# Kernel tuning notes

Measured on AMD Instinct MI355X. Metric: run time of the kernel, lower is better.

The kernel has to match this reference:

```python
import jax, jax.numpy as jnp
import numpy as np

D = 1024          # input_dim
H = 16            # num_heads
S = 2             # scalar
MAX_LEN = 2048
HEAD_DIM = D // H // S      # 32
DV = D // H                 # 64, value head dim
SCALING = (D // H) ** -0.5


def setup_inputs() -> dict:
    key = jax.random.key(0)
    k1, k2, k3, k4, k5, k6 = jax.random.split(key, 6)
    L, B = 2046, 4
    input_tensor = jax.random.normal(k1, (L, B, D), dtype=jnp.float32)
    # k_v_proj: Linear(MAX_LEN, MAX_LEN // S); bias exists but is unused in forward
    w_kv = jax.random.normal(k2, (MAX_LEN // S, MAX_LEN), dtype=jnp.float32) / np.sqrt(MAX_LEN)
    # q_proj: Linear(D, D // S)
    w_q = jax.random.normal(k3, (D // S, D), dtype=jnp.float32) / np.sqrt(D)
    b_q = jax.random.normal(k4, (D // S,), dtype=jnp.float32) * 0.01
    # out_proj: Linear(D, D)
    w_out = jax.random.normal(k5, (D, D), dtype=jnp.float32) / np.sqrt(D)
    b_out = jax.random.normal(k6, (D,), dtype=jnp.float32) * 0.01
    return {"input_tensor": input_tensor, "w_kv": w_kv, "w_q": w_q,
            "b_q": b_q, "w_out": w_out, "b_out": b_out}


def reference(input_tensor, w_kv, w_q, b_q, w_out, b_out):
    L, B, _ = input_tensor.shape
    P = L // S + 1                       # projected (low-rank) sequence length
    X = jnp.transpose(input_tensor, (1, 0, 2))        # [B, L, D]
    q = X @ w_q.T + b_q                                # [B, L, D/S]
    Wp = w_kv.T[:L, :P]                                # [L, P] sequence projection
    v = jnp.einsum('bld,lp->bdp', X, Wp)               # [B, D, P]
    k = jnp.einsum('blc,lp->bcp', q, Wp)               # [B, D/S, P]
    q = q * SCALING
    # q: b l (h d) -> b h l d
    qh = q.reshape(B, L, H, HEAD_DIM).transpose(0, 2, 1, 3)
    # k: b (d h) p -> b h d p   (d outer, h inner in the channel split)
    kh = k.reshape(B, HEAD_DIM, H, P).transpose(0, 2, 1, 3)
    # v: b (d h) p -> b h p d
    vh = v.reshape(B, DV, H, P).transpose(0, 2, 3, 1)
    attn = jnp.einsum('bhld,bhdp->bhlp', qh, kh)       # [B, H, L, P]
    attn = jax.nn.softmax(attn.astype(jnp.float32), axis=-1).astype(attn.dtype)
    out = jnp.einsum('bhlp,bhpd->bhld', attn, vh)      # [B, H, L, DV]
    # (b h) l d -> b l (d h): d outer, h inner in concat
    out = out.transpose(0, 2, 3, 1).reshape(B, L, D)
    out = out @ w_out.T + b_out                        # [B, L, D]
    return jnp.transpose(out, (1, 0, 2))               # [L, B, D]
```

## Files before the change

kernel.cpp:

```cpp
#include <hip/hip_runtime.h>
#include <hip/hip_bf16.h>

typedef long long i64;
typedef unsigned int uint;
using u16 = unsigned short;
using f32x4  = __attribute__((ext_vector_type(4))) float;
using bf16x8 = __attribute__((ext_vector_type(8))) short;
using u32x4  = __attribute__((ext_vector_type(4))) uint;
using u16x4  = __attribute__((ext_vector_type(4))) u16;

#define QSCALE 0.18033688011112042f

#if __has_builtin(__builtin_amdgcn_exp2f)
#define EXP2(x) __builtin_amdgcn_exp2f(x)
#else
#define EXP2(x) __builtin_exp2f(x)
#endif

__device__ __forceinline__ u16 f2b(float x) {
    uint u = __float_as_uint(x);
    return (u16)((u + 0x7FFFu + ((u >> 16) & 1u)) >> 16);
}
__device__ __forceinline__ float b2f(u16 h) {
    return __uint_as_float((uint)h << 16);
}
__device__ __forceinline__ uint cvt_pk_bf16(float lo, float hi) {
    uint r;
    asm("v_cvt_pk_bf16_f32 %0, %1, %2" : "=v"(r) : "v"(lo), "v"(hi));
    return r;
}

__global__ __launch_bounds__(256) void conv_pad(
    const float* __restrict__ src, u16* __restrict__ dst,
    int M_valid, int K_valid, int kshift, int s_row)
{
    i64 i = (i64)blockIdx.x * 256 + threadIdx.x;
    int m = (int)(i >> (kshift - 2));
    int k = ((int)(i & ((1 << (kshift - 2)) - 1))) << 2;
    u16x4 hv;
    #pragma unroll
    for (int j = 0; j < 4; ++j) {
        int kk = k + j;
        float x = (m < M_valid && kk < K_valid) ? src[(i64)m * s_row + kk] : 0.f;
        hv[j] = f2b(x);
    }
    *(u16x4*)(dst + ((i64)m << kshift) + k) = hv;
}

__global__ __launch_bounds__(256) void conv_wout_perm(
    const float* __restrict__ w, u16* __restrict__ dst)
{
    int i = blockIdx.x * 256 + threadIdx.x;
    int n = i >> 8, kp4 = (i & 255) << 2;
    u16x4 hv;
    #pragma unroll
    for (int j = 0; j < 4; ++j) {
        int kp = kp4 + j;
        hv[j] = f2b(w[((i64)n << 10) + ((kp & 63) << 4) + (kp >> 6)]);
    }
    *(u16x4*)(dst + ((i64)n << 10) + kp4) = hv;
}

__global__ __launch_bounds__(256) void build_kvA(
    const u16* __restrict__ Xb, const u16* __restrict__ qu,
    u16* __restrict__ dst)
{
    const int b = blockIdx.z, r0 = blockIdx.y * 64, l0 = blockIdx.x * 64;
    const int tid = threadIdx.x;
    __shared__ float ts[64][65];
    #pragma unroll
    for (int t = 0; t < 16; ++t) {
        int idx = t * 256 + tid;
        int ch = idx & 63, lr = idx >> 6;
        int lg = l0 + lr;
        float v = 0.f;
        if (lg < 2046) {
            if (r0 < 1024) v = b2f(Xb[((i64)lg * 4 + b) * 1024 + (r0 + ch)]);
            else           v = b2f(qu[((i64)lg * 4 + b) * 512 + (r0 - 1024 + ch)]);
        }
        ts[lr][ch] = v;
    }
    __syncthreads();
    #pragma unroll
    for (int t = 0; t < 16; ++t) {
        int idx = t * 256 + tid;
        int ll = idx & 63, rl = idx >> 6;
        dst[((i64)b * 1536 + r0 + rl) * 2048 + l0 + ll] = f2b(ts[ll][rl]);
    }
}

template<int MODE>
__global__ __launch_bounds__(256) void gemm_bf16(
    const u16* __restrict__ A, i64 a_bs,
    const u16* __restrict__ Bm,
    float* __restrict__ C, const float* __restrict__ bias,
    u16* __restrict__ x0, u16* __restrict__ x1,
    int Krow, int KT, int M_valid)
{
    __shared__ __align__(16) u16 As[4096], Bs[8192];
    const int tid = threadIdx.x, lane = tid & 63, w = tid >> 6;
    const int fr = lane & 15, g = lane >> 4;

    const int fid = blockIdx.x;
    const int xcd = fid & 7, s = fid >> 3;
    int nb, mb, bz;
    if (MODE == 0)      { nb = s & 3; mb = xcd * 16 + (s >> 2); bz = 0; }
    else if (MODE == 1) { nb = s & 7; int pr = xcd * 12 + (s >> 3); bz = pr / 24; mb = pr % 24; }
    else                { nb = s & 7; int pr = xcd * 16 + (s >> 3); bz = pr >> 5; mb = pr & 31; }

    const int srow = tid >> 3, sch = tid & 7;
    const int scol = (sch ^ (srow & 7)) << 3;
    const u16* Asrc = A + (i64)bz * a_bs + ((i64)mb * 64 + srow) * Krow + scol;
    const u16* Bsrc = Bm + ((i64)nb * 128 + srow) * Krow + scol;
    char* Adst = (char*)As + srow * 128 + sch * 16;
    char* Bdst = (char*)Bs + srow * 128 + sch * 16;

    f32x4 acc[2][4];
    #pragma unroll
    for (int i = 0; i < 2; ++i)
        #pragma unroll
        for (int j = 0; j < 4; ++j)
            acc[i][j] = (f32x4){0.f, 0.f, 0.f, 0.f};

    u32x4 st[6];
    st[0] = *(const u32x4*)(Asrc);
    st[1] = *(const u32x4*)(Asrc + (i64)32 * Krow);
    #pragma unroll
    for (int it = 0; it < 4; ++it)
        st[2 + it] = *(const u32x4*)(Bsrc + (i64)(it * 32) * Krow);

    const int wr = (w & 1) * 32, wc = (w >> 1) * 64;

    for (int kt = 0; kt < KT; ++kt) {
        __syncthreads();
        *(u32x4*)(Adst) = st[0];
        *(u32x4*)(Adst + 32 * 128) = st[1];
        #pragma unroll
        for (int it = 0; it < 4; ++it)
            *(u32x4*)(Bdst + it * 32 * 128) = st[2 + it];
        __syncthreads();
        if (kt + 1 < KT) {
            st[0] = *(const u32x4*)(Asrc + (kt + 1) * 64);
            st[1] = *(const u32x4*)(Asrc + (i64)32 * Krow + (kt + 1) * 64);
            #pragma unroll
            for (int it = 0; it < 4; ++it)
                st[2 + it] = *(const u32x4*)(Bsrc + (i64)(it * 32) * Krow
                                                  + (kt + 1) * 64);
        }
        #pragma unroll
        for (int half = 0; half < 2; ++half) {
            bf16x8 ah[2], bh[4];
            #pragma unroll
            for (int mi = 0; mi < 2; ++mi) {
                int rr = wr + mi * 16 + fr;
                ah[mi] = *(const bf16x8*)((const char*)As + rr * 128
                                          + (((half * 4 + g) ^ (rr & 7)) << 4));
            }
            #pragma unroll
            for (int ni = 0; ni < 4; ++ni) {
                int rr = wc + ni * 16 + fr;
                bh[ni] = *(const bf16x8*)((const char*)Bs + rr * 128
                                          + (((half * 4 + g) ^ (rr & 7)) << 4));
            }
            #pragma unroll
            for (int mi = 0; mi < 2; ++mi)
                #pragma unroll
                for (int ni = 0; ni < 4; ++ni)
                    acc[mi][ni] = __builtin_amdgcn_mfma_f32_16x16x32_bf16(
                        ah[mi], bh[ni], acc[mi][ni], 0, 0, 0);
        }
    }

    #pragma unroll
    for (int mi = 0; mi < 2; ++mi)
        #pragma unroll
        for (int ni = 0; ni < 4; ++ni) {
            int gm0 = mb * 64 + wr + mi * 16 + g * 4;
            int gn  = nb * 128 + wc + ni * 16 + fr;
            #pragma unroll
            for (int r = 0; r < 4; ++r) {
                int gm = gm0 + r;
                float val = acc[mi][ni][r];
                if (MODE == 0) {
                    x0[(i64)gm * 512 + gn] = f2b(val + bias[gn]);
                } else if (MODE == 1) {
                    if (gm < 1024) {
                        int e = gm >> 4, hh = gm & 15;
                        i64 so = ((i64)(bz * 16 + hh) * 64 + e) * 1024
                               + (gn & ~31) + (((gn >> 2) & 3) << 3)
                               + (gn & 3) + (((gn >> 4) & 1) << 2);
                        x1[so] = f2b(val);
                    } else {
                        int c2 = gm - 1024, d = c2 >> 4, hh = c2 & 15;
                        x0[((i64)(bz * 16 + hh) * 1024 + gn) * 32 + d] = f2b(val);
                    }
                } else {
                    if (gm < M_valid)
                        C[(i64)bz * 1024 + (i64)gm * 4096 + gn] = val + bias[gn];
                }
            }
        }
}

__global__ __launch_bounds__(256) void attn_mfma(
    const u16* __restrict__ qu, const u16* __restrict__ kT,
    const u16* __restrict__ vT, u16* __restrict__ attA)
{
    const int g0 = blockIdx.x;
    const int xcd = g0 & 7, sub = g0 >> 3;
    const int lblk = sub & 15;
    const int bh = xcd + ((sub >> 4) << 3);
    const int b = bh >> 4, h = bh & 15;
    const int tid = threadIdx.x, lane = tid & 63, w = tid >> 6;
    const int fr = lane & 15, g = lane >> 4;
    const int l0 = lblk * 128 + w * 32;

    __shared__ __align__(16) u16 kbuf[2][2560];
    __shared__ __align__(16) u16 vbuf[2][4608];

    bf16x8 aq[2];
    #pragma unroll
    for (int mf = 0; mf < 2; ++mf)
        aq[mf] = *(const bf16x8*)(qu + ((i64)((l0 + mf * 16 + fr) * 4 + b) * 512
                                        + h * 32 + g * 8));

    const f32x4 zf = {0.f, 0.f, 0.f, 0.f};

    const int sr = tid >> 2, sc = tid & 3;
    const u16* ksrc = kT + (i64)bh * 32768 + sr * 32 + sc * 8;
    char* kdst = (char*)&kbuf[0][0] + sr * 80 + sc * 16;
    const u16* vsrc = vT + (i64)bh * 65536 + (i64)sr * 1024 + sc * 8;
    char* vdst = (char*)&vbuf[0][0] + sr * 144 + sc * 16;

    *(u32x4*)kdst = *(const u32x4*)ksrc;
    *(u32x4*)vdst = *(const u32x4*)vsrc;
    *(u32x4*)(vdst + 64) = *(const u32x4*)(vsrc + 32);
    __syncthreads();

    float l_part[2] = {0.f, 0.f};
    f32x4 o[2][4];
    #pragma unroll
    for (int mf = 0; mf < 2; ++mf)
        #pragma unroll
        for (int nf = 0; nf < 4; ++nf)
            o[mf][nf] = zf;

    for (int t = 0; t < 16; ++t) {
        const int cur = t & 1;
        const int tn = (t < 15) ? t + 1 : 15;

        u32x4 knx  = *(const u32x4*)(ksrc + tn * 2048);
        u32x4 vnx0 = *(const u32x4*)(vsrc + tn * 64);
        u32x4 vnx1 = *(const u32x4*)(vsrc + tn * 64 + 32);

        const char* kc_ = (const char*)&kbuf[cur][0];
        f32x4 s[2][4];
        __builtin_amdgcn_s_setprio(1);
        #pragma unroll
        for (int nf = 0; nf < 4; ++nf) {
            bf16x8 ak = *(const bf16x8*)(kc_ + (nf * 16 + fr) * 80 + g * 16);
            s[0][nf] = __builtin_amdgcn_mfma_f32_16x16x32_bf16(ak, aq[0], zf, 0, 0, 0);
            s[1][nf] = __builtin_amdgcn_mfma_f32_16x16x32_bf16(ak, aq[1], zf, 0, 0, 0);
        }
        __builtin_amdgcn_s_setprio(0);

        u32x4 ppk[2][2];
        #pragma unroll
        for (int mf = 0; mf < 2; ++mf)
            #pragma unroll
            for (int nf = 0; nf < 4; ++nf) {
                float p_[4];
                #pragma unroll
                for (int r = 0; r < 4; ++r) p_[r] = EXP2(QSCALE * s[mf][nf][r]);
                l_part[mf] += (p_[0] + p_[1]) + (p_[2] + p_[3]);
                ppk[mf][nf >> 1][(nf & 1) * 2 + 0] = cvt_pk_bf16(p_[0], p_[1]);
                ppk[mf][nf >> 1][(nf & 1) * 2 + 1] = cvt_pk_bf16(p_[2], p_[3]);
            }

        {
            const int nb_ = cur ^ 1;
            *(u32x4*)(kdst + nb_ * 5120) = knx;
            *(u32x4*)(vdst + nb_ * 9216) = vnx0;
            *(u32x4*)(vdst + nb_ * 9216 + 64) = vnx1;
        }

        const char* vc_ = (const char*)&vbuf[cur][0];
        __builtin_amdgcn_s_setprio(1);
        #pragma unroll
        for (int ks = 0; ks < 2; ++ks) {
            bf16x8 ap0 = __builtin_bit_cast(bf16x8, ppk[0][ks]);
            bf16x8 ap1 = __builtin_bit_cast(bf16x8, ppk[1][ks]);
            #pragma unroll
            for (int nf = 0; nf < 4; ++nf) {
                bf16x8 bv = *(const bf16x8*)(vc_ + (nf * 16 + fr) * 144
                                                 + ks * 64 + g * 16);
                o[0][nf] = __builtin_amdgcn_mfma_f32_16x16x32_bf16(ap0, bv, o[0][nf], 0, 0, 0);
                o[1][nf] = __builtin_amdgcn_mfma_f32_16x16x32_bf16(ap1, bv, o[1][nf], 0, 0, 0);
            }
        }
        __builtin_amdgcn_s_setprio(0);

        __syncthreads();
    }

    #pragma unroll
    for (int mf = 0; mf < 2; ++mf) {
        l_part[mf] += __shfl_xor(l_part[mf], 16);
        l_part[mf] += __shfl_xor(l_part[mf], 32);
    }
    #pragma unroll
    for (int mf = 0; mf < 2; ++mf)
        #pragma unroll
        for (int r = 0; r < 4; ++r) {
            int l = l0 + mf * 16 + g * 4 + r;
            float tot = __shfl(l_part[mf], g * 4 + r);
            if (l < 2046) {
                float inv = 1.f / tot;
                #pragma unroll
                for (int nf = 0; nf < 4; ++nf)
                    attA[((i64)b * 2048 + l) * 1024 + h * 64 + nf * 16 + fr]
                        = f2b(o[mf][nf][r] * inv);
            }
        }
}

extern "C" void kernel_launch(void* const* d_in, const int* in_sizes, int n_in,
                              void* d_out, int out_size, void* d_ws, size_t ws_size,
                              hipStream_t stream) {
    const float* input = (const float*)d_in[0];
    const float* w_kv  = (const float*)d_in[1];
    const float* w_q   = (const float*)d_in[2];
    const float* b_q   = (const float*)d_in[3];
    const float* w_out = (const float*)d_in[4];
    const float* b_out = (const float*)d_in[5];
    float* out = (float*)d_out;

    char* W = (char*)d_ws;
    u16* Xb      = (u16*)(W + 16777216);
    u16* qu      = (u16*)(W + 33554432);
    u16* wq_b    = (u16*)(W + 41943040);
    u16* wkv_b   = (u16*)(W + 42991616);
    u16* wout_b  = (u16*)(W + 47185920);
    u16* kvA     = (u16*)(W + 49283072);
    u16* kT      = (u16*)(W + 74448896);
    u16* vT      = (u16*)(W + 78643200);
    u16* attA    = (u16*)(W + 87031808);

    dim3 blk(256);

    conv_pad<<<8192, blk, 0, stream>>>(input, Xb, 8184, 1024, 10, 1024);
    conv_pad<<<512,  blk, 0, stream>>>(w_q, wq_b, 512, 1024, 10, 1024);
    conv_pad<<<2048, blk, 0, stream>>>(w_kv, wkv_b, 1024, 2046, 11, 2048);
    conv_wout_perm<<<1024, blk, 0, stream>>>(w_out, wout_b);

    gemm_bf16<0><<<dim3(512), blk, 0, stream>>>(
        Xb, 0, wq_b, nullptr, b_q, qu, nullptr, 1024, 16, 8192);

    build_kvA<<<dim3(32, 24, 4), blk, 0, stream>>>(Xb, qu, kvA);

    gemm_bf16<1><<<dim3(768), blk, 0, stream>>>(
        kvA, (i64)1536 * 2048, wkv_b, nullptr, nullptr, kT, vT, 2048, 32, 1536);

    attn_mfma<<<dim3(1024), blk, 0, stream>>>(qu, kT, vT, attA);

    gemm_bf16<2><<<dim3(1024), blk, 0, stream>>>(
        attA, (i64)2048 * 1024, wout_b, out, b_out, nullptr, nullptr, 1024, 16, 2046);
}
```

Baseline: 182.1 us.

## Double-buffer LDS tiles in bf16 GEMM with one barrier per k-step

Splits the shared-memory A/B tiles into two buffers and unrolls the k-loop by two. Global loads for tiles two steps ahead are issued into registers while MFMAs run on the current buffer. This cuts the two __syncthreads per k-step to a single lgkmcnt wait plus barrier, so loads, LDS writes and compute overlap more. LDS use doubles to about 48KB per block, which can lower occupancy. The loop also assumes KT is even.

```diff
diff --git a/kernel.cpp b/kernel.cpp
--- a/kernel.cpp
+++ b/kernel.cpp
@@ -97,7 +97,7 @@
     u16* __restrict__ x0, u16* __restrict__ x1,
     int Krow, int KT, int M_valid)
 {
-    __shared__ __align__(16) u16 As[4096], Bs[8192];
+    __shared__ __align__(16) u16 As[2][4096], Bs[2][8192];
     const int tid = threadIdx.x, lane = tid & 63, w = tid >> 6;
     const int fr = lane & 15, g = lane >> 4;
 
@@ -112,8 +112,27 @@
     const int scol = (sch ^ (srow & 7)) << 3;
     const u16* Asrc = A + (i64)bz * a_bs + ((i64)mb * 64 + srow) * Krow + scol;
     const u16* Bsrc = Bm + ((i64)nb * 128 + srow) * Krow + scol;
-    char* Adst = (char*)As + srow * 128 + sch * 16;
-    char* Bdst = (char*)Bs + srow * 128 + sch * 16;
+    char* Ad = (char*)&As[0][0] + srow * 128 + sch * 16;
+    char* Bd = (char*)&Bs[0][0] + srow * 128 + sch * 16;
+
+#define GLOADS(dst, t) do { \
+        dst[0] = *(const u32x4*)(Asrc + (i64)(t) * 64); \
+        dst[1] = *(const u32x4*)(Asrc + (i64)32 * Krow + (i64)(t) * 64); \
+        dst[2] = *(const u32x4*)(Bsrc + (i64)(t) * 64); \
+        dst[3] = *(const u32x4*)(Bsrc + (i64)32 * Krow + (i64)(t) * 64); \
+        dst[4] = *(const u32x4*)(Bsrc + (i64)64 * Krow + (i64)(t) * 64); \
+        dst[5] = *(const u32x4*)(Bsrc + (i64)96 * Krow + (i64)(t) * 64); \
+    } while (0)
+#define DSWRITE(srcv, p) do { \
+        *(u32x4*)(Ad + (p) * 8192)             = srcv[0]; \
+        *(u32x4*)(Ad + (p) * 8192 + 32 * 128)  = srcv[1]; \
+        *(u32x4*)(Bd + (p) * 16384)            = srcv[2]; \
+        *(u32x4*)(Bd + (p) * 16384 + 32 * 128) = srcv[3]; \
+        *(u32x4*)(Bd + (p) * 16384 + 64 * 128) = srcv[4]; \
+        *(u32x4*)(Bd + (p) * 16384 + 96 * 128) = srcv[5]; \
+    } while (0)
+#define GFENCE() do { asm volatile("s_waitcnt lgkmcnt(0)" ::: "memory"); \
+                      __builtin_amdgcn_s_barrier(); } while (0)
 
     f32x4 acc[2][4];
     #pragma unroll
@@ -122,45 +141,23 @@
         for (int j = 0; j < 4; ++j)
             acc[i][j] = (f32x4){0.f, 0.f, 0.f, 0.f};
 
-    u32x4 st[6];
-    st[0] = *(const u32x4*)(Asrc);
-    st[1] = *(const u32x4*)(Asrc + (i64)32 * Krow);
-    #pragma unroll
-    for (int it = 0; it < 4; ++it)
-        st[2 + it] = *(const u32x4*)(Bsrc + (i64)(it * 32) * Krow);
-
     const int wr = (w & 1) * 32, wc = (w >> 1) * 64;
 
-    for (int kt = 0; kt < KT; ++kt) {
-        __syncthreads();
-        *(u32x4*)(Adst) = st[0];
-        *(u32x4*)(Adst + 32 * 128) = st[1];
-        #pragma unroll
-        for (int it = 0; it < 4; ++it)
-            *(u32x4*)(Bdst + it * 32 * 128) = st[2 + it];
-        __syncthreads();
-        if (kt + 1 < KT) {
-            st[0] = *(const u32x4*)(Asrc + (kt + 1) * 64);
-            st[1] = *(const u32x4*)(Asrc + (i64)32 * Krow + (kt + 1) * 64);
-            #pragma unroll
-            for (int it = 0; it < 4; ++it)
-                st[2 + it] = *(const u32x4*)(Bsrc + (i64)(it * 32) * Krow
-                                                  + (kt + 1) * 64);
-        }
+    auto mfma_phase = [&](int p) {
+        const char* Ab = (const char*)&As[0][0] + p * 8192;
+        const char* Bb = (const char*)&Bs[0][0] + p * 16384;
         #pragma unroll
         for (int half = 0; half < 2; ++half) {
             bf16x8 ah[2], bh[4];
             #pragma unroll
             for (int mi = 0; mi < 2; ++mi) {
                 int rr = wr + mi * 16 + fr;
-                ah[mi] = *(const bf16x8*)((const char*)As + rr * 128
-                                          + (((half * 4 + g) ^ (rr & 7)) << 4));
+                ah[mi] = *(const bf16x8*)(Ab + rr * 128 + (((half * 4 + g) ^ (rr & 7)) << 4));
             }
             #pragma unroll
             for (int ni = 0; ni < 4; ++ni) {
                 int rr = wc + ni * 16 + fr;
-                bh[ni] = *(const bf16x8*)((const char*)Bs + rr * 128
-                                          + (((half * 4 + g) ^ (rr & 7)) << 4));
+                bh[ni] = *(const bf16x8*)(Bb + rr * 128 + (((half * 4 + g) ^ (rr & 7)) << 4));
             }
             #pragma unroll
             for (int mi = 0; mi < 2; ++mi)
@@ -169,7 +166,27 @@
                     acc[mi][ni] = __builtin_amdgcn_mfma_f32_16x16x32_bf16(
                         ah[mi], bh[ni], acc[mi][ni], 0, 0, 0);
         }
-    }
+    };
+
+    u32x4 stE[6], stO[6], tmp[6];
+    GLOADS(tmp, 0);
+    GLOADS(stE, 1);
+    DSWRITE(tmp, 0);
+    GFENCE();
+
+    for (int kt = 0; kt < KT; kt += 2) {
+        mfma_phase(0);
+        if (kt + 2 < KT) GLOADS(stO, kt + 2);
+        DSWRITE(stE, 1);
+        GFENCE();
+        mfma_phase(1);
+        if (kt + 3 < KT) GLOADS(stE, kt + 3);
+        if (kt + 2 < KT) DSWRITE(stO, 0);
+        GFENCE();
+    }
+#undef GLOADS
+#undef DSWRITE
+#undef GFENCE
 
     #pragma unroll
     for (int mi = 0; mi < 2; ++mi)
```

After: 191.5 us. +5.1%, slower.

## Merge conversion kernels into one launch and remap GEMM tiles per XCD

Applied to the files above, without the earlier changes.

The four fp32-to-bf16 conversion kernels are merged into one launch that dispatches on block index, which removes three kernel launches and the gaps between them. The GEMM block-to-tile mapping is also changed so that each XCD (chiplet) owns a fixed N-column block of the weight matrix, improving L2 reuse of B tiles within a chiplet. The cost is that A tiles are now spread across XCDs instead of being shared, so the locality gain depends on which operand dominates traffic.

```diff
diff --git a/kernel.cpp b/kernel.cpp
--- a/kernel.cpp
+++ b/kernel.cpp
@@ -30,11 +30,11 @@
     return r;
 }
 
-__global__ __launch_bounds__(256) void conv_pad(
-    const float* __restrict__ src, u16* __restrict__ dst,
+__device__ __forceinline__ void conv_pad_dev(
+    int bid, const float* __restrict__ src, u16* __restrict__ dst,
     int M_valid, int K_valid, int kshift, int s_row)
 {
-    i64 i = (i64)blockIdx.x * 256 + threadIdx.x;
+    i64 i = (i64)bid * 256 + threadIdx.x;
     int m = (int)(i >> (kshift - 2));
     int k = ((int)(i & ((1 << (kshift - 2)) - 1))) << 2;
     u16x4 hv;
@@ -46,11 +46,10 @@
     }
     *(u16x4*)(dst + ((i64)m << kshift) + k) = hv;
 }
-
-__global__ __launch_bounds__(256) void conv_wout_perm(
-    const float* __restrict__ w, u16* __restrict__ dst)
-{
-    int i = blockIdx.x * 256 + threadIdx.x;
+__device__ __forceinline__ void conv_wout_dev(
+    int bid, const float* __restrict__ w, u16* __restrict__ dst)
+{
+    int i = bid * 256 + threadIdx.x;
     int n = i >> 8, kp4 = (i & 255) << 2;
     u16x4 hv;
     #pragma unroll
@@ -59,6 +58,18 @@
         hv[j] = f2b(w[((i64)n << 10) + ((kp & 63) << 4) + (kp >> 6)]);
     }
     *(u16x4*)(dst + ((i64)n << 10) + kp4) = hv;
+}
+__global__ __launch_bounds__(256) void conv_all(
+    const float* __restrict__ X, const float* __restrict__ wq,
+    const float* __restrict__ wkv, const float* __restrict__ wout,
+    u16* __restrict__ Xb, u16* __restrict__ wq_b,
+    u16* __restrict__ wkv_b, u16* __restrict__ wout_b)
+{
+    const int bid = blockIdx.x;
+    if (bid < 8192)       conv_pad_dev(bid, X, Xb, 8184, 1024, 10, 1024);
+    else if (bid < 8704)  conv_pad_dev(bid - 8192, wq, wq_b, 512, 1024, 10, 1024);
+    else if (bid < 10752) conv_pad_dev(bid - 8704, wkv, wkv_b, 1024, 2046, 11, 2048);
+    else                  conv_wout_dev(bid - 10752, wout, wout_b);
 }
 
 __global__ __launch_bounds__(256) void build_kvA(
@@ -104,9 +115,9 @@
     const int fid = blockIdx.x;
     const int xcd = fid & 7, s = fid >> 3;
     int nb, mb, bz;
-    if (MODE == 0)      { nb = s & 3; mb = xcd * 16 + (s >> 2); bz = 0; }
-    else if (MODE == 1) { nb = s & 7; int pr = xcd * 12 + (s >> 3); bz = pr / 24; mb = pr % 24; }
-    else                { nb = s & 7; int pr = xcd * 16 + (s >> 3); bz = pr >> 5; mb = pr & 31; }
+    if (MODE == 0)      { nb = xcd >> 1; mb = (xcd & 1) * 64 + s; bz = 0; }
+    else if (MODE == 1) { nb = xcd; mb = s % 24; bz = s / 24; }
+    else                { nb = xcd; mb = s & 31; bz = s >> 5; }
 
     const int srow = tid >> 3, sch = tid & 7;
     const int scol = (sch ^ (srow & 7)) << 3;
@@ -348,10 +359,8 @@
 
     dim3 blk(256);
 
-    conv_pad<<<8192, blk, 0, stream>>>(input, Xb, 8184, 1024, 10, 1024);
-    conv_pad<<<512,  blk, 0, stream>>>(w_q, wq_b, 512, 1024, 10, 1024);
-    conv_pad<<<2048, blk, 0, stream>>>(w_kv, wkv_b, 1024, 2046, 11, 2048);
-    conv_wout_perm<<<1024, blk, 0, stream>>>(w_out, wout_b);
+    conv_all<<<dim3(11776), blk, 0, stream>>>(
+        input, w_q, w_kv, w_out, Xb, wq_b, wkv_b, wout_b);
 
     gemm_bf16<0><<<dim3(512), blk, 0, stream>>>(
         Xb, 0, wq_b, nullptr, b_q, qu, nullptr, 1024, 16, 8192);
```

After: 169.2 us. 7.1% less time.
